# Kernel optimization log

Measured on AMD Instinct MI355X. Metric: run time of the kernel, lower is better.

Reference implementation:

```python
import jax, jax.numpy as jnp
import numpy as np

DIM = 2048
SEQ = 8192
NUM_HEADS = 16
PROJ_DIM = DIM // 4  # proj_ratio = 4.0
EPS = 1e-5


def setup_inputs() -> dict:
    key = jax.random.key(0)
    ks = jax.random.split(key, 8)
    s = 0.02  # param init scale
    return {
        "x": jax.random.normal(ks[0], (SEQ, DIM), jnp.float32),
        "q": jax.random.normal(ks[1], (1, DIM), jnp.float32),
        "W_kv": jax.random.normal(ks[2], (2 * DIM, DIM), jnp.float32) * s,
        "b_kv": jax.random.normal(ks[3], (2 * DIM,), jnp.float32) * s,
        "W_p1": jax.random.normal(ks[4], (PROJ_DIM, DIM), jnp.float32) * s,
        "b_p1": jax.random.normal(ks[5], (PROJ_DIM,), jnp.float32) * s,
        "W_p2": jax.random.normal(ks[6], (DIM, PROJ_DIM), jnp.float32) * s,
        "b_p2": jax.random.normal(ks[7], (DIM,), jnp.float32) * s,
        "ln_w": jnp.ones((PROJ_DIM,), jnp.float32),
        "ln_b": jnp.zeros((PROJ_DIM,), jnp.float32),
    }


def reference(x, q, W_kv, b_kv, W_p1, b_p1, W_p2, b_p2, ln_w, ln_b):
    seq, dim = x.shape
    h = NUM_HEADS
    d = dim // h

    # kv projection: [s, 2*dim]; split '(n h d)' with n leading -> k = first dim cols
    kv = x @ W_kv.T + b_kv
    k = kv[:, :dim].reshape(seq, h, d).transpose(1, 0, 2)   # [h, s, d]
    v = kv[:, dim:].reshape(seq, h, d).transpose(1, 0, 2)   # [h, s, d]
    qh = q.reshape(h, 1, d)                                  # '1 (h d) -> h 1 d'

    # single-query attention (qk_norm=False -> Identity norms)
    attn = jnp.einsum('hqd,hkd->hqk', qh, k) / jnp.sqrt(jnp.asarray(d, x.dtype))
    attn = jax.nn.softmax(attn, axis=-1)                     # [h, 1, s]
    x1 = jnp.einsum('hqk,hkd->hqd', attn, v)                 # [h, 1, d]
    x1 = x1.transpose(1, 0, 2).reshape(1, dim)               # 'h s d -> s (h d)'

    # proj MLP: proj1 -> LayerNorm -> relu -> proj2
    h1 = x1 @ W_p1.T + b_p1                                  # [1, proj_dim]
    mu = jnp.mean(h1, axis=-1, keepdims=True)
    var = jnp.mean(jnp.square(h1 - mu), axis=-1, keepdims=True)
    h1 = (h1 - mu) / jnp.sqrt(var + EPS) * ln_w + ln_b
    x1 = jax.nn.relu(h1) @ W_p2.T + b_p2                     # [1, dim]

    # residual broadcast: [s, dim] + [1, dim]
    return x + x1
```

## Files before the change

kernel.cpp:

```cpp
#include <hip/hip_runtime.h>
#include <math.h>

#define SEQ   8192
#define DIM   2048
#define NH    16
#define DH    128
#define PD    512

static constexpr float LN_EPS = 1e-5f;
static constexpr float SCALE  = 0.08838834764831845f;

static constexpr size_t OFF_QW   = 0;
static constexpr size_t OFF_QB   = OFF_QW + 32768;
static constexpr size_t OFF_SMP  = OFF_QB + 16;
static constexpr size_t OFF_ELOG = OFF_SMP + 128;
static constexpr size_t OFF_PCTX = OFF_ELOG + 131072;
static constexpr size_t OFF_CTX  = OFF_PCTX + 64*32768;
static constexpr size_t OFF_X1   = OFF_CTX + 32768;
static constexpr size_t OFF_H1R  = OFF_X1 + 2048;
static constexpr size_t OFF_X1F  = OFF_H1R + 512;

__global__ __launch_bounds__(256) void k_prep(const float* __restrict__ q,
                                              const float* __restrict__ Wkv,
                                              const float* __restrict__ bkv,
                                              float* __restrict__ qW,
                                              float* __restrict__ qb,
                                              float* __restrict__ smp) {
    int t = threadIdx.x;
    int h = blockIdx.x >> 4, jc = blockIdx.x & 15;
    int col = t & 127, kh = t >> 7;
    int j = jc * 128 + col;
    const float* w  = Wkv + (size_t)(h * DH + kh * 64) * DIM + j;
    const float* qh = q + h * DH + kh * 64;
    float acc = 0.f;
#pragma unroll 16
    for (int d = 0; d < 64; ++d)
        acc += qh[d] * w[(size_t)d * DIM];
    __shared__ float part[128];
    if (kh) part[col] = acc;
    __syncthreads();
    if (!kh) qW[h * DIM + j] = acc + part[col];
    if (jc == 0 && t < 64) {
        float p = q[h*DH + t] * bkv[h*DH + t] + q[h*DH + 64 + t] * bkv[h*DH + 64 + t];
        for (int off = 32; off; off >>= 1) p += __shfl_down(p, off);
        if (t == 0) qb[h] = p;
    }
    if (blockIdx.x == 0 && t < 128) smp[t] = 0.f;
}

__global__ __launch_bounds__(256) void k_logits(const float* __restrict__ x,
                                                const float* __restrict__ qW,
                                                const float* __restrict__ qb,
                                                float* __restrict__ elog,
                                                float* __restrict__ smp) {
    const int t = threadIdx.x, g = blockIdx.x;
    const int s0 = blockIdx.y * 16;
    const int j0 = t * 8;
    float4 qw0[8], qw1[8];
#pragma unroll
    for (int hh = 0; hh < 8; ++hh) {
        const float* base = qW + (size_t)(g * 8 + hh) * DIM + j0;
        qw0[hh] = *(const float4*)base;
        qw1[hh] = *(const float4*)(base + 4);
    }
    __shared__ float part[4][16][8];
    __shared__ float esh[16][8];
    const int lane = t & 63, w = t >> 6;
    const int head = ((lane & 1) << 2) | (lane & 2) | ((lane >> 2) & 1);
    for (int r = 0; r < 16; ++r) {
        const float* xr = x + (size_t)(s0 + r) * DIM + j0;
        float4 xa = *(const float4*)xr;
        float4 xb = *(const float4*)(xr + 4);
        float p[8];
#pragma unroll
        for (int hh = 0; hh < 8; ++hh) {
            p[hh] = xa.x*qw0[hh].x + xa.y*qw0[hh].y + xa.z*qw0[hh].z + xa.w*qw0[hh].w
                  + xb.x*qw1[hh].x + xb.y*qw1[hh].y + xb.z*qw1[hh].z + xb.w*qw1[hh].w;
        }
#pragma unroll
        for (int k = 0; k < 3; ++k) {
            const int m = 1 << k, n = 8 >> k;
            const bool hi = (lane >> k) & 1;
#pragma unroll
            for (int i = 0; i < (n >> 1); ++i) {
                float a = p[i], b = p[i + (n >> 1)];
                float send = hi ? a : b;
                float recv = __shfl_xor(send, m);
                p[i] = (hi ? b : a) + recv;
            }
        }
        float v = p[0];
        v += __shfl_xor(v, 8);
        v += __shfl_xor(v, 16);
        v += __shfl_xor(v, 32);
        if (lane < 8) part[w][r][head] = v;
    }
    __syncthreads();
    if (t < 128) {
        int r = t >> 3, hh = t & 7, h = g * 8 + hh;
        float sum = part[0][r][hh] + part[1][r][hh] + part[2][r][hh] + part[3][r][hh];
        float e = __expf((sum + qb[h]) * SCALE);
        elog[(size_t)h * SEQ + s0 + r] = e;
        esh[r][hh] = e;
    }
    __syncthreads();
    if (t < 8) {
        float s = 0.f;
#pragma unroll
        for (int r = 0; r < 16; ++r) s += esh[r][t];
        atomicAdd(&smp[(g * 8 + t) * 8 + (blockIdx.y & 7)], s);
    }
}

__global__ __launch_bounds__(256) void k_ctx(const float* __restrict__ x,
                                             const float* __restrict__ elog,
                                             const float* __restrict__ smp,
                                             float* __restrict__ pctx) {
    int jc = blockIdx.x & 3, sc = blockIdx.x >> 2, t = threadIdx.x;
    int s0 = sc * 128;
    int j = jc * 512 + t * 2;
    __shared__ float inv_s[NH];
    __shared__ float att[128][NH];
    if (t < NH) {
        float S = 0.f;
#pragma unroll
        for (int i = 0; i < 8; ++i) S += smp[t * 8 + i];
        inv_s[t] = 1.0f / S;
    }
    __syncthreads();
    for (int i = t; i < 128 * NH; i += 256) {
        int h = i >> 7, r = i & 127;
        att[r][h] = elog[(size_t)h * SEQ + s0 + r] * inv_s[h];
    }
    __syncthreads();
    float2 acc[NH];
#pragma unroll
    for (int h = 0; h < NH; ++h) acc[h] = make_float2(0.f, 0.f);
    for (int r = 0; r < 128; ++r) {
        float2 xv = *(const float2*)&x[(size_t)(s0 + r) * DIM + j];
        const float4* ar = (const float4*)att[r];
        float4 a0 = ar[0], a1 = ar[1], a2 = ar[2], a3 = ar[3];
        float aa[NH];
        *(float4*)&aa[0] = a0; *(float4*)&aa[4]  = a1;
        *(float4*)&aa[8] = a2; *(float4*)&aa[12] = a3;
#pragma unroll
        for (int h = 0; h < NH; ++h) {
            acc[h].x += aa[h] * xv.x;
            acc[h].y += aa[h] * xv.y;
        }
    }
#pragma unroll
    for (int h = 0; h < NH; ++h)
        *(float2*)&pctx[((size_t)(sc * NH + h)) * DIM + j] = acc[h];
}

__global__ __launch_bounds__(256) void k_ctxred(const float* __restrict__ pctx,
                                                float* __restrict__ ctx) {
    int idx = blockIdx.x * 256 + threadIdx.x;
    float s = 0.f;
#pragma unroll 8
    for (int sc = 0; sc < 64; ++sc)
        s += pctx[(size_t)sc * (NH * DIM) + idx];
    ctx[idx] = s;
}

__global__ __launch_bounds__(256) void k_x1(const float* __restrict__ Wkv,
                                            const float* __restrict__ bkv,
                                            const float* __restrict__ ctx,
                                            float* __restrict__ x1) {
    int row = blockIdx.x * 4 + (threadIdx.x >> 6);
    int lane = threadIdx.x & 63;
    const float* w = Wkv + (size_t)(DIM + row) * DIM;
    const float* c = ctx + (row >> 7) * DIM;
    float acc = 0.f;
#pragma unroll
    for (int k = 0; k < 8; ++k) {
        int j = k * 256 + lane * 4;
        float4 wv = *(const float4*)&w[j];
        float4 cv = *(const float4*)&c[j];
        acc += wv.x*cv.x + wv.y*cv.y + wv.z*cv.z + wv.w*cv.w;
    }
    for (int off = 32; off; off >>= 1) acc += __shfl_xor(acc, off);
    if (lane == 0) x1[row] = acc + bkv[DIM + row];
}

__global__ __launch_bounds__(256) void k_h1(const float* __restrict__ Wp1,
                                            const float* __restrict__ bp1,
                                            const float* __restrict__ x1,
                                            float* __restrict__ h1raw) {
    int row = blockIdx.x * 4 + (threadIdx.x >> 6);
    int lane = threadIdx.x & 63;
    const float* w = Wp1 + (size_t)row * DIM;
    float acc = 0.f;
#pragma unroll
    for (int k = 0; k < 8; ++k) {
        int j = k * 256 + lane * 4;
        float4 wv = *(const float4*)&w[j];
        float4 cv = *(const float4*)&x1[j];
        acc += wv.x*cv.x + wv.y*cv.y + wv.z*cv.z + wv.w*cv.w;
    }
    for (int off = 32; off; off >>= 1) acc += __shfl_xor(acc, off);
    if (lane == 0) h1raw[row] = acc + bp1[row];
}

__global__ __launch_bounds__(256) void k_x1f(const float* __restrict__ Wp2,
                                             const float* __restrict__ bp2,
                                             const float* __restrict__ h1raw,
                                             const float* __restrict__ lnw,
                                             const float* __restrict__ lnb,
                                             float* __restrict__ x1f) {
    int row = blockIdx.x * 4 + (threadIdx.x >> 6);
    int lane = threadIdx.x & 63;
    int j = lane * 8;
    float4 va = *(const float4*)&h1raw[j];
    float4 vb = *(const float4*)&h1raw[j + 4];
    float s = va.x + va.y + va.z + va.w + vb.x + vb.y + vb.z + vb.w;
    for (int off = 32; off; off >>= 1) s += __shfl_xor(s, off);
    float mu = s * (1.0f / PD);
    float dx[8];
    dx[0]=va.x-mu; dx[1]=va.y-mu; dx[2]=va.z-mu; dx[3]=va.w-mu;
    dx[4]=vb.x-mu; dx[5]=vb.y-mu; dx[6]=vb.z-mu; dx[7]=vb.w-mu;
    float s2 = 0.f;
#pragma unroll
    for (int i = 0; i < 8; ++i) s2 += dx[i] * dx[i];
    for (int off = 32; off; off >>= 1) s2 += __shfl_xor(s2, off);
    float rstd = rsqrtf(s2 * (1.0f / PD) + LN_EPS);
    float4 lw0 = *(const float4*)&lnw[j], lw1 = *(const float4*)&lnw[j + 4];
    float4 lb0 = *(const float4*)&lnb[j], lb1 = *(const float4*)&lnb[j + 4];
    float hln[8];
    hln[0]=fmaxf(dx[0]*rstd*lw0.x+lb0.x,0.f); hln[1]=fmaxf(dx[1]*rstd*lw0.y+lb0.y,0.f);
    hln[2]=fmaxf(dx[2]*rstd*lw0.z+lb0.z,0.f); hln[3]=fmaxf(dx[3]*rstd*lw0.w+lb0.w,0.f);
    hln[4]=fmaxf(dx[4]*rstd*lw1.x+lb1.x,0.f); hln[5]=fmaxf(dx[5]*rstd*lw1.y+lb1.y,0.f);
    hln[6]=fmaxf(dx[6]*rstd*lw1.z+lb1.z,0.f); hln[7]=fmaxf(dx[7]*rstd*lw1.w+lb1.w,0.f);
    const float* w = Wp2 + (size_t)row * PD + j;
    float4 w0 = *(const float4*)w, w1 = *(const float4*)(w + 4);
    float acc = w0.x*hln[0] + w0.y*hln[1] + w0.z*hln[2] + w0.w*hln[3]
              + w1.x*hln[4] + w1.y*hln[5] + w1.z*hln[6] + w1.w*hln[7];
    for (int off = 32; off; off >>= 1) acc += __shfl_xor(acc, off);
    if (lane == 0) x1f[row] = acc + bp2[row];
}

__global__ __launch_bounds__(256) void k_out(const float* __restrict__ x,
                                             const float* __restrict__ x1f,
                                             float* __restrict__ out) {
    size_t i = (size_t)blockIdx.x * 512 + threadIdx.x;
    float4 xv = ((const float4*)x)[i];
    float4 a  = ((const float4*)x1f)[(int)(i & 511)];
    ((float4*)out)[i] = make_float4(xv.x + a.x, xv.y + a.y, xv.z + a.z, xv.w + a.w);
    size_t i2 = i + 256;
    float4 xv2 = ((const float4*)x)[i2];
    float4 a2  = ((const float4*)x1f)[(int)(i2 & 511)];
    ((float4*)out)[i2] = make_float4(xv2.x + a2.x, xv2.y + a2.y, xv2.z + a2.z, xv2.w + a2.w);
}

extern "C" void kernel_launch(void* const* d_in, const int* in_sizes, int n_in,
                              void* d_out, int out_size, void* d_ws, size_t ws_size,
                              hipStream_t stream) {
    const float* x    = (const float*)d_in[0];
    const float* q    = (const float*)d_in[1];
    const float* Wkv  = (const float*)d_in[2];
    const float* bkv  = (const float*)d_in[3];
    const float* Wp1  = (const float*)d_in[4];
    const float* bp1  = (const float*)d_in[5];
    const float* Wp2  = (const float*)d_in[6];
    const float* bp2  = (const float*)d_in[7];
    const float* lnw  = (const float*)d_in[8];
    const float* lnb  = (const float*)d_in[9];
    float* out = (float*)d_out;
    float* ws  = (float*)d_ws;

    float* qW    = ws + OFF_QW;
    float* qb    = ws + OFF_QB;
    float* smp   = ws + OFF_SMP;
    float* elog  = ws + OFF_ELOG;
    float* pctx  = ws + OFF_PCTX;
    float* ctx   = ws + OFF_CTX;
    float* x1    = ws + OFF_X1;
    float* h1raw = ws + OFF_H1R;
    float* x1f   = ws + OFF_X1F;

    k_prep  <<<256, 256, 0, stream>>>(q, Wkv, bkv, qW, qb, smp);
    k_logits<<<dim3(2, 512), 256, 0, stream>>>(x, qW, qb, elog, smp);
    k_ctx   <<<256, 256, 0, stream>>>(x, elog, smp, pctx);
    k_ctxred<<<128, 256, 0, stream>>>(pctx, ctx);
    k_x1    <<<512, 256, 0, stream>>>(Wkv, bkv, ctx, x1);
    k_h1    <<<128, 256, 0, stream>>>(Wp1, bp1, x1, h1raw);
    k_x1f   <<<512, 256, 0, stream>>>(Wp2, bp2, h1raw, lnw, lnb, x1f);
    k_out   <<<8192, 256, 0, stream>>>(x, x1f, out);
}
```

Before: 244.5 us.

## Compute attention logits with bf16 MFMA and transpose logit layout

Rewrites the logits kernel so each block handles 16 sequence rows for all 16 heads using bf16 16x16x32 MFMA, with the q·W_k vector precomputed and stored in bf16. The shuffle-based reduction and the two-block split over heads go away, so x is read once instead of twice. Logits are stored sequence-major so the context kernel reads them contiguously. The context kernel now uses 64-row chunks across twice as many blocks, which doubles the partial-context buffer and the reduction length. Converting x and qW to bf16 adds rounding error to the softmax logits.

```diff
diff --git a/kernel.cpp b/kernel.cpp
--- a/kernel.cpp
+++ b/kernel.cpp
@@ -10,12 +10,15 @@
 static constexpr float LN_EPS = 1e-5f;
 static constexpr float SCALE  = 0.08838834764831845f;
 
-static constexpr size_t OFF_QW   = 0;
-static constexpr size_t OFF_QB   = OFF_QW + 32768;
-static constexpr size_t OFF_SMP  = OFF_QB + 16;
-static constexpr size_t OFF_ELOG = OFF_SMP + 128;
+typedef __bf16 bf16x8 __attribute__((ext_vector_type(8)));
+typedef float  f32x4  __attribute__((ext_vector_type(4)));
+
+static constexpr size_t OFF_QB   = 0;
+static constexpr size_t OFF_SMP  = 16;
+static constexpr size_t OFF_QWB  = 528;
+static constexpr size_t OFF_ELOG = OFF_QWB + 16384;
 static constexpr size_t OFF_PCTX = OFF_ELOG + 131072;
-static constexpr size_t OFF_CTX  = OFF_PCTX + 64*32768;
+static constexpr size_t OFF_CTX  = OFF_PCTX + 128*32768;
 static constexpr size_t OFF_X1   = OFF_CTX + 32768;
 static constexpr size_t OFF_H1R  = OFF_X1 + 2048;
 static constexpr size_t OFF_X1F  = OFF_H1R + 512;
@@ -23,7 +26,7 @@
 __global__ __launch_bounds__(256) void k_prep(const float* __restrict__ q,
                                               const float* __restrict__ Wkv,
                                               const float* __restrict__ bkv,
-                                              float* __restrict__ qW,
+                                              __bf16* __restrict__ qWb,
                                               float* __restrict__ qb,
                                               float* __restrict__ smp) {
     int t = threadIdx.x;
@@ -39,106 +42,92 @@
     __shared__ float part[128];
     if (kh) part[col] = acc;
     __syncthreads();
-    if (!kh) qW[h * DIM + j] = acc + part[col];
+    if (!kh) qWb[h * DIM + j] = (__bf16)(acc + part[col]);
     if (jc == 0 && t < 64) {
         float p = q[h*DH + t] * bkv[h*DH + t] + q[h*DH + 64 + t] * bkv[h*DH + 64 + t];
         for (int off = 32; off; off >>= 1) p += __shfl_down(p, off);
         if (t == 0) qb[h] = p;
     }
-    if (blockIdx.x == 0 && t < 128) smp[t] = 0.f;
+    if (blockIdx.x == 0) { smp[t] = 0.f; smp[t + 256] = 0.f; }
 }
 
 __global__ __launch_bounds__(256) void k_logits(const float* __restrict__ x,
-                                                const float* __restrict__ qW,
+                                                const __bf16* __restrict__ qWb,
                                                 const float* __restrict__ qb,
-                                                float* __restrict__ elog,
+                                                float* __restrict__ elogT,
                                                 float* __restrict__ smp) {
-    const int t = threadIdx.x, g = blockIdx.x;
-    const int s0 = blockIdx.y * 16;
-    const int j0 = t * 8;
-    float4 qw0[8], qw1[8];
-#pragma unroll
-    for (int hh = 0; hh < 8; ++hh) {
-        const float* base = qW + (size_t)(g * 8 + hh) * DIM + j0;
-        qw0[hh] = *(const float4*)base;
-        qw1[hh] = *(const float4*)(base + 4);
-    }
-    __shared__ float part[4][16][8];
-    __shared__ float esh[16][8];
-    const int lane = t & 63, w = t >> 6;
-    const int head = ((lane & 1) << 2) | (lane & 2) | ((lane >> 2) & 1);
-    for (int r = 0; r < 16; ++r) {
-        const float* xr = x + (size_t)(s0 + r) * DIM + j0;
-        float4 xa = *(const float4*)xr;
-        float4 xb = *(const float4*)(xr + 4);
-        float p[8];
-#pragma unroll
-        for (int hh = 0; hh < 8; ++hh) {
-            p[hh] = xa.x*qw0[hh].x + xa.y*qw0[hh].y + xa.z*qw0[hh].z + xa.w*qw0[hh].w
-                  + xb.x*qw1[hh].x + xb.y*qw1[hh].y + xb.z*qw1[hh].z + xb.w*qw1[hh].w;
-        }
-#pragma unroll
-        for (int k = 0; k < 3; ++k) {
-            const int m = 1 << k, n = 8 >> k;
-            const bool hi = (lane >> k) & 1;
-#pragma unroll
-            for (int i = 0; i < (n >> 1); ++i) {
-                float a = p[i], b = p[i + (n >> 1)];
-                float send = hi ? a : b;
-                float recv = __shfl_xor(send, m);
-                p[i] = (hi ? b : a) + recv;
-            }
-        }
-        float v = p[0];
-        v += __shfl_xor(v, 8);
-        v += __shfl_xor(v, 16);
-        v += __shfl_xor(v, 32);
-        if (lane < 8) part[w][r][head] = v;
-    }
-    __syncthreads();
-    if (t < 128) {
-        int r = t >> 3, hh = t & 7, h = g * 8 + hh;
-        float sum = part[0][r][hh] + part[1][r][hh] + part[2][r][hh] + part[3][r][hh];
-        float e = __expf((sum + qb[h]) * SCALE);
-        elog[(size_t)h * SEQ + s0 + r] = e;
-        esh[r][hh] = e;
-    }
-    __syncthreads();
-    if (t < 8) {
-        float s = 0.f;
-#pragma unroll
-        for (int r = 0; r < 16; ++r) s += esh[r][t];
-        atomicAdd(&smp[(g * 8 + t) * 8 + (blockIdx.y & 7)], s);
-    }
+    const int t = threadIdx.x;
+    const int w = t >> 6, lane = t & 63;
+    const int r = lane & 15, quad = lane >> 4;
+    const int s0 = blockIdx.x * 16;
+    __shared__ float dpart[4][64][4];
+    __shared__ float hsum[NH];
+    if (t < NH) hsum[t] = 0.f;
+
+    const float*  xrow = x + (size_t)(s0 + r) * DIM + quad * 8;
+    const __bf16* brow = qWb + r * DIM + quad * 8;
+    const int kbase = w * 512;
+
+    f32x4 acc = {0.f, 0.f, 0.f, 0.f};
+#pragma unroll 4
+    for (int i = 0; i < 16; ++i) {
+        int k = kbase + i * 32;
+        float4 xa = *(const float4*)(xrow + k);
+        float4 xb = *(const float4*)(xrow + k + 4);
+        bf16x8 af;
+        af[0] = (__bf16)xa.x; af[1] = (__bf16)xa.y;
+        af[2] = (__bf16)xa.z; af[3] = (__bf16)xa.w;
+        af[4] = (__bf16)xb.x; af[5] = (__bf16)xb.y;
+        af[6] = (__bf16)xb.z; af[7] = (__bf16)xb.w;
+        bf16x8 bf = *(const bf16x8*)(brow + k);
+        acc = __builtin_amdgcn_mfma_f32_16x16x32_bf16(af, bf, acc, 0, 0, 0);
+    }
+    dpart[w][lane][0] = acc[0];
+    dpart[w][lane][1] = acc[1];
+    dpart[w][lane][2] = acc[2];
+    dpart[w][lane][3] = acc[3];
+    __syncthreads();
+
+    {
+        const int lane2 = t & 63, reg = t >> 6;
+        const int h = lane2 & 15, sl = (lane2 >> 4) * 4 + reg;
+        float v = dpart[0][lane2][reg] + dpart[1][lane2][reg]
+                + dpart[2][lane2][reg] + dpart[3][lane2][reg];
+        float e = __expf((v + qb[h]) * SCALE);
+        elogT[(size_t)(s0 + sl) * NH + h] = e;
+        atomicAdd(&hsum[h], e);
+    }
+    __syncthreads();
+    if (t < NH) atomicAdd(&smp[t * 32 + (blockIdx.x & 31)], hsum[t]);
 }
 
 __global__ __launch_bounds__(256) void k_ctx(const float* __restrict__ x,
-                                             const float* __restrict__ elog,
+                                             const float* __restrict__ elogT,
                                              const float* __restrict__ smp,
                                              float* __restrict__ pctx) {
     int jc = blockIdx.x & 3, sc = blockIdx.x >> 2, t = threadIdx.x;
-    int s0 = sc * 128;
+    int s0 = sc * 64;
     int j = jc * 512 + t * 2;
     __shared__ float inv_s[NH];
-    __shared__ float att[128][NH];
+    __shared__ float att[64][NH];
     if (t < NH) {
         float S = 0.f;
 #pragma unroll
-        for (int i = 0; i < 8; ++i) S += smp[t * 8 + i];
+        for (int i = 0; i < 32; ++i) S += smp[t * 32 + i];
         inv_s[t] = 1.0f / S;
     }
     __syncthreads();
-    for (int i = t; i < 128 * NH; i += 256) {
-        int h = i >> 7, r = i & 127;
-        att[r][h] = elog[(size_t)h * SEQ + s0 + r] * inv_s[h];
+    for (int i = t; i < 64 * NH; i += 256) {
+        int rr = i >> 4, h = i & 15;
+        att[rr][h] = elogT[(size_t)(s0 + rr) * NH + h] * inv_s[h];
     }
     __syncthreads();
     float2 acc[NH];
 #pragma unroll
     for (int h = 0; h < NH; ++h) acc[h] = make_float2(0.f, 0.f);
-    for (int r = 0; r < 128; ++r) {
-        float2 xv = *(const float2*)&x[(size_t)(s0 + r) * DIM + j];
-        const float4* ar = (const float4*)att[r];
+    for (int rr = 0; rr < 64; ++rr) {
+        float2 xv = *(const float2*)&x[(size_t)(s0 + rr) * DIM + j];
+        const float4* ar = (const float4*)att[rr];
         float4 a0 = ar[0], a1 = ar[1], a2 = ar[2], a3 = ar[3];
         float aa[NH];
         *(float4*)&aa[0] = a0; *(float4*)&aa[4]  = a1;
@@ -159,7 +148,7 @@
     int idx = blockIdx.x * 256 + threadIdx.x;
     float s = 0.f;
 #pragma unroll 8
-    for (int sc = 0; sc < 64; ++sc)
+    for (int sc = 0; sc < 128; ++sc)
         s += pctx[(size_t)sc * (NH * DIM) + idx];
     ctx[idx] = s;
 }
@@ -269,19 +258,19 @@
     float* out = (float*)d_out;
     float* ws  = (float*)d_ws;
 
-    float* qW    = ws + OFF_QW;
-    float* qb    = ws + OFF_QB;
-    float* smp   = ws + OFF_SMP;
-    float* elog  = ws + OFF_ELOG;
-    float* pctx  = ws + OFF_PCTX;
-    float* ctx   = ws + OFF_CTX;
-    float* x1    = ws + OFF_X1;
-    float* h1raw = ws + OFF_H1R;
-    float* x1f   = ws + OFF_X1F;
-
-    k_prep  <<<256, 256, 0, stream>>>(q, Wkv, bkv, qW, qb, smp);
-    k_logits<<<dim3(2, 512), 256, 0, stream>>>(x, qW, qb, elog, smp);
-    k_ctx   <<<256, 256, 0, stream>>>(x, elog, smp, pctx);
+    float*  qb    = ws + OFF_QB;
+    float*  smp   = ws + OFF_SMP;
+    __bf16* qWb   = (__bf16*)(ws + OFF_QWB);
+    float*  elogT = ws + OFF_ELOG;
+    float*  pctx  = ws + OFF_PCTX;
+    float*  ctx   = ws + OFF_CTX;
+    float*  x1    = ws + OFF_X1;
+    float*  h1raw = ws + OFF_H1R;
+    float*  x1f   = ws + OFF_X1F;
+
+    k_prep  <<<256, 256, 0, stream>>>(q, Wkv, bkv, qWb, qb, smp);
+    k_logits<<<512, 256, 0, stream>>>(x, qWb, qb, elogT, smp);
+    k_ctx   <<<512, 256, 0, stream>>>(x, elogT, smp, pctx);
     k_ctxred<<<128, 256, 0, stream>>>(pctx, ctx);
     k_x1    <<<512, 256, 0, stream>>>(Wkv, bkv, ctx, x1);
     k_h1    <<<128, 256, 0, stream>>>(Wp1, bp1, x1, h1raw);
```

Result: faster. 222.2 us (-9.1%).
